# Performance work log

Hardware: AMD Instinct MI355X
Metric: run time of the kernel (lower is better)

The kernel has to match this reference:

```python
import jax, jax.numpy as jnp
import numpy as np

S = 2048      # seq_len
H = 32        # num_heads
G = 8         # num_groups (KV heads)
D = 128       # head_dim
HPG = H // G  # heads per group
MODEL = H * D


def setup_inputs() -> dict:
    rng = jax.random.key(0)
    ks = jax.random.split(rng, 6)
    return {
        "query": jax.random.normal(ks[0], (S, H, D), jnp.float32),
        "key":   jax.random.normal(ks[1], (S, G, D), jnp.float32),
        "value": jax.random.normal(ks[2], (S, G, D), jnp.float32),
        "mask":  jnp.zeros((S, S), jnp.float32),
        "w_out": jax.random.normal(ks[3], (MODEL, MODEL), jnp.float32) * (MODEL ** -0.5),
        "b_out": jnp.zeros((MODEL,), jnp.float32),
    }


def reference(query, key, value, mask, w_out, b_out):
    # NOTE: the original torch module prepares `mask` but never applies it to
    # the attention scores; we faithfully reproduce that (mask is unused).
    scale = D ** -0.5
    # [S,H,D] -> [H,S,D] -> [G,HPG,S,D]; head h = g*HPG + i (torch .view split)
    q = query.transpose(1, 0, 2).reshape(G, HPG, S, D)
    k = key.transpose(1, 0, 2)    # [G,S,D]
    v = value.transpose(1, 0, 2)  # [G,S,D]
    scores = jnp.einsum('ghqd,gkd->ghqk', q, k) * scale  # [G,HPG,S,S]
    attn = jax.nn.softmax(scores, axis=-1)
    out = jnp.einsum('ghqk,gkd->ghqd', attn, v)          # [G,HPG,S,D]
    # [G,HPG,S,D] -> [H,S,D] -> [S,H,D] -> [S, H*D]
    out = out.reshape(H, S, D).transpose(1, 0, 2).reshape(S, MODEL)
    out = out @ w_out.T + b_out                           # out_proj (Linear)
    return out.reshape(S, H, D)
```

## Files before the change

### kernel.cpp

```cpp
#include <hip/hip_runtime.h>
#include <hip/hip_bf16.h>
#include <stdint.h>

constexpr int S_ = 2048, H_ = 32, G_ = 8, HPG_ = 4, D_ = 128, MODEL_ = 4096;

typedef __attribute__((ext_vector_type(4))) float f32x4;
typedef __attribute__((ext_vector_type(16))) float f32x16;
typedef __attribute__((ext_vector_type(8))) short bf16x8;
typedef __attribute__((ext_vector_type(4))) short bf16x4;

__device__ inline unsigned short f2bf(float f) {
  unsigned u = __float_as_uint(f);
  u += 0x7FFFu + ((u >> 16) & 1u);
  return (unsigned short)(u >> 16);
}

__device__ inline unsigned cvt_pk_bf16(float lo, float hi) {
  unsigned r;
  asm("v_cvt_pk_bf16_f32 %0, %1, %2" : "=v"(r) : "v"(lo), "v"(hi));
  return r;
}

__device__ inline void gload_lds16(const void* g, void* l) {
  __builtin_amdgcn_global_load_lds(
      (const __attribute__((address_space(1))) unsigned int*)g,
      (__attribute__((address_space(3))) unsigned int*)l,
      16, 0, 0);
}

__global__ __launch_bounds__(256) void cvt_f32_to_bf16(
    const float* __restrict__ in, unsigned short* __restrict__ out, int n4) {
  int i = blockIdx.x * 256 + threadIdx.x;
  if (i < n4) {
    float4 v = reinterpret_cast<const float4*>(in)[i];
    bf16x4 o;
    o[0] = f2bf(v.x); o[1] = f2bf(v.y); o[2] = f2bf(v.z); o[3] = f2bf(v.w);
    reinterpret_cast<bf16x4*>(out)[i] = o;
  }
}

__global__ __launch_bounds__(256) void cvt_k_kernel(
    const float* __restrict__ in, unsigned short* __restrict__ out) {
  int i = blockIdx.x * 256 + threadIdx.x;
  int d4 = i & 31, g = (i >> 5) & 7, s = i >> 8;
  float4 v = reinterpret_cast<const float4*>(in)[i];
  bf16x4 o;
  o[0] = f2bf(v.x); o[1] = f2bf(v.y); o[2] = f2bf(v.z); o[3] = f2bf(v.w);
  reinterpret_cast<bf16x4*>(out)[(g * S_ + s) * 32 + d4] = o;
}

__global__ __launch_bounds__(256) void cvt_v_kernel(
    const float* __restrict__ in, unsigned short* __restrict__ out) {
  __shared__ float t[64][33];
  int s0 = blockIdx.x * 64, d0 = blockIdx.y * 32, g = blockIdx.z;
  int tid = threadIdx.x;
#pragma unroll
  for (int p = 0; p < 2; ++p) {
    int idx = p * 256 + tid;
    int s = idx >> 3, dq = (idx & 7) * 4;
    float4 v = *reinterpret_cast<const float4*>(
        in + ((size_t)(s0 + s) * G_ + g) * D_ + d0 + dq);
    t[s][dq] = v.x; t[s][dq + 1] = v.y; t[s][dq + 2] = v.z; t[s][dq + 3] = v.w;
  }
  __syncthreads();
  int d = tid >> 3, sq = (tid & 7) * 8;
  bf16x8 o;
#pragma unroll
  for (int j = 0; j < 8; ++j) o[j] = f2bf(t[sq + j][d]);
  *reinterpret_cast<bf16x8*>(out + ((size_t)g * D_ + d0 + d) * S_ + s0 + sq) = o;
}

constexpr int QB2 = 128, KVB = 32, NT = S_ / KVB;
constexpr float RTHR = 8.0f;

__global__ __launch_bounds__(256, 2) void attn32_kernel(
    const float* __restrict__ q, const unsigned short* __restrict__ kb,
    const unsigned short* __restrict__ vtb, unsigned short* __restrict__ aout) {
  __shared__ __align__(16) char smem[49152];

  const int qt = blockIdx.x, h = blockIdx.y;
  const int g = h >> 2;
  const int tid = threadIdx.x, w = tid >> 6, lane = tid & 63;
  const int l31 = lane & 31, hi = lane >> 5;

  const float scale = 0.08838834764831845f;
  bf16x8 qf[8];
  const int qrow = qt * QB2 + w * 32 + l31;
  {
    const float* qp = q + ((size_t)qrow * H_ + h) * D_;
#pragma unroll
    for (int c = 0; c < 8; ++c) {
      const float* p0 = qp + c * 16 + hi * 8;
      float4 a = *(const float4*)p0;
      float4 b = *(const float4*)(p0 + 4);
      bf16x8 f;
      f[0] = f2bf(a.x * scale); f[1] = f2bf(a.y * scale);
      f[2] = f2bf(a.z * scale); f[3] = f2bf(a.w * scale);
      f[4] = f2bf(b.x * scale); f[5] = f2bf(b.y * scale);
      f[6] = f2bf(b.z * scale); f[7] = f2bf(b.w * scale);
      qf[c] = f;
    }
  }

  int ks_kv[2], ks_d[2], vs_d[2], vs_kv[2];
#pragma unroll
  for (int hh = 0; hh < 2; ++hh) {
    int p = w * 1024 + hh * 4096 + lane * 16;
    int kvr = p >> 8;
    ks_kv[hh] = kvr;
    ks_d[hh] = ((p & 255) ^ ((kvr & 7) << 4)) >> 1;
    int dr = p >> 6;
    vs_d[hh] = dr;
    vs_kv[hh] = ((p & 63) ^ (((dr >> 1) & 3) << 4)) >> 1;
  }
  const unsigned short* kg = kb + (size_t)g * S_ * D_;
  const unsigned short* vg = vtb + (size_t)g * D_ * S_;

  auto stage = [&](int t, int buf) {
    int kv0 = t * KVB;
    char* Kd = smem + buf * 16384;
    char* Vd = smem + buf * 16384 + 8192;
#pragma unroll
    for (int hh = 0; hh < 2; ++hh) {
      gload_lds16(kg + (size_t)(kv0 + ks_kv[hh]) * D_ + ks_d[hh],
                  Kd + w * 1024 + hh * 4096);
      gload_lds16(vg + (size_t)vs_d[hh] * S_ + kv0 + vs_kv[hh],
                  Vd + w * 1024 + hh * 4096);
    }
  };

  f32x16 of[4];
#pragma unroll
  for (int i = 0; i < 4; ++i) of[i] = (f32x16)0.f;
  float m = -1e30f, l = 0.f;

  stage(0, 0);
  stage(1, 1);

  for (int t = 0; t < NT; ++t) {
    const int buf = t % 3;
    if (t + 1 < NT) asm volatile("s_waitcnt vmcnt(4)" ::: "memory");
    else            asm volatile("s_waitcnt vmcnt(0)" ::: "memory");
    __builtin_amdgcn_s_barrier();
    if (t + 2 < NT) stage(t + 2, (t + 2) % 3);

    const char* Kd = smem + buf * 16384;
    const char* Vd = smem + buf * 16384 + 8192;

    f32x16 s0 = (f32x16)0.f, s1 = (f32x16)0.f;
    __builtin_amdgcn_s_setprio(1);
#pragma unroll
    for (int c = 0; c < 8; ++c) {
      unsigned off = ((unsigned)(l31 * 256 + c * 32 + hi * 16)) ^
                     ((unsigned)(l31 & 7) << 4);
      bf16x8 kf = *(const bf16x8*)(Kd + off);
      if (c & 1)
        s1 = __builtin_amdgcn_mfma_f32_32x32x16_bf16(kf, qf[c], s1, 0, 0, 0);
      else
        s0 = __builtin_amdgcn_mfma_f32_32x32x16_bf16(kf, qf[c], s0, 0, 0, 0);
    }
    __builtin_amdgcn_s_setprio(0);
    f32x16 sv = s0 + s1;

    float tmax = sv[0];
#pragma unroll
    for (int r = 1; r < 16; ++r) tmax = fmaxf(tmax, sv[r]);
    tmax = fmaxf(tmax, __shfl_xor(tmax, 32));
    if (__any(tmax > m + RTHR)) {
      float mnew = fmaxf(m, tmax);
      float alpha = __expf(m - mnew);
#pragma unroll
      for (int i = 0; i < 4; ++i)
#pragma unroll
        for (int r = 0; r < 16; ++r) of[i][r] *= alpha;
      l *= alpha;
      m = mnew;
    }
    float pv[16];
    float sum = 0.f;
#pragma unroll
    for (int r = 0; r < 16; ++r) { pv[r] = __expf(sv[r] - m); sum += pv[r]; }
    sum += __shfl_xor(sum, 32);
    l += sum;

    unsigned pk[8];
#pragma unroll
    for (int b = 0; b < 8; ++b) pk[b] = cvt_pk_bf16(pv[2 * b], pv[2 * b + 1]);
    bf16x8 pf[2];
#pragma unroll
    for (int kc = 0; kc < 2; ++kc) {
      auto sA = __builtin_amdgcn_permlane32_swap(pk[kc * 4 + 0], pk[kc * 4 + 2],
                                                 false, false);
      auto sB = __builtin_amdgcn_permlane32_swap(pk[kc * 4 + 1], pk[kc * 4 + 3],
                                                 false, false);
      unsigned fr[4] = {(unsigned)sA[0], (unsigned)sB[0],
                        (unsigned)sA[1], (unsigned)sB[1]};
      __builtin_memcpy(&pf[kc], fr, 16);
    }

    __builtin_amdgcn_s_setprio(1);
#pragma unroll
    for (int db = 0; db < 4; ++db) {
      int d = db * 32 + l31;
#pragma unroll
      for (int kc = 0; kc < 2; ++kc) {
        unsigned off = ((unsigned)(d * 64 + kc * 32 + hi * 16)) ^
                       ((unsigned)((d >> 1) & 3) << 4);
        bf16x8 vf = *(const bf16x8*)(Vd + off);
        of[db] = __builtin_amdgcn_mfma_f32_32x32x16_bf16(vf, pf[kc], of[db], 0, 0, 0);
      }
    }
    __builtin_amdgcn_s_setprio(0);
  }

  __syncthreads();
  float inv = 1.0f / l;
  unsigned short* Ol = (unsigned short*)smem;
  const int ql = w * 32 + l31;
#pragma unroll
  for (int db = 0; db < 4; ++db) {
#pragma unroll
    for (int rp = 0; rp < 8; ++rp) {
      int r0 = rp * 2;
      int d0 = db * 32 + (r0 & 3) + 8 * (r0 >> 2) + 4 * hi;
      unsigned pkv = cvt_pk_bf16(of[db][r0] * inv, of[db][r0 + 1] * inv);
      unsigned off = ((unsigned)(ql * 256 + d0 * 2)) ^ ((unsigned)(ql & 7) << 4);
      *(unsigned*)((char*)Ol + off) = pkv;
    }
  }
  __syncthreads();
  const size_t obase = ((size_t)qt * QB2) * MODEL_ + (size_t)h * D_;
#pragma unroll
  for (int pass = 0; pass < 8; ++pass) {
    int row = pass * 16 + (tid >> 4);
    int c = tid & 15;
    unsigned off = ((unsigned)(row * 256 + c * 16)) ^ ((unsigned)(row & 7) << 4);
    bf16x8 vv = *(const bf16x8*)((char*)Ol + off);
    *(bf16x8*)(aout + obase + (size_t)row * MODEL_ + c * 8) = vv;
  }
}

constexpr int BM = 128, BN = 128, BK = 64;

__global__ __launch_bounds__(256, 2) void gemm_bt_bias(
    const unsigned short* __restrict__ A, const unsigned short* __restrict__ B,
    const float* __restrict__ bias, float* __restrict__ C) {
  __shared__ unsigned short As[BM * BK];
  __shared__ unsigned short Bs[BN * BK];

  const int tid = threadIdx.x;
  const int w = tid >> 6, lane = tid & 63;
  const int wr = w >> 1, wc = w & 1;
  const int r16 = lane & 15, g4 = lane >> 4;
  const int row0 = blockIdx.y * BM, col0 = blockIdx.x * BN;

  f32x4 acc[4][4];
#pragma unroll
  for (int m = 0; m < 4; ++m)
#pragma unroll
    for (int n = 0; n < 4; ++n) acc[m][n] = (f32x4)0.f;

  for (int kt = 0; kt < MODEL_ / BK; ++kt) {
    const int k0 = kt * BK;
    __syncthreads();
#pragma unroll
    for (int j = 0; j < 4; ++j) {
      int chunk = w * 4 + j;
      int sb = chunk * 1024 + lane * 16;
      int srow = sb >> 7;
      int lb = sb ^ ((srow & 7) << 4);
      int kk = (lb & 127) >> 1;
      gload_lds16(A + (size_t)(row0 + srow) * MODEL_ + k0 + kk,
                  (char*)As + chunk * 1024);
      gload_lds16(B + (size_t)(col0 + srow) * MODEL_ + k0 + kk,
                  (char*)Bs + chunk * 1024);
    }
    asm volatile("s_waitcnt vmcnt(0)" ::: "memory");
    __syncthreads();

#pragma unroll
    for (int kc = 0; kc < 2; ++kc) {
      bf16x8 af[4], bfr[4];
#pragma unroll
      for (int m = 0; m < 4; ++m) {
        int row = wr * 64 + m * 16 + r16;
        unsigned off = ((unsigned)(row * 128 + (kc * 32 + g4 * 8) * 2)) ^ ((row & 7) << 4);
        af[m] = *(bf16x8*)((char*)As + off);
      }
#pragma unroll
      for (int n = 0; n < 4; ++n) {
        int row = wc * 64 + n * 16 + r16;
        unsigned off = ((unsigned)(row * 128 + (kc * 32 + g4 * 8) * 2)) ^ ((row & 7) << 4);
        bfr[n] = *(bf16x8*)((char*)Bs + off);
      }
#pragma unroll
      for (int m = 0; m < 4; ++m)
#pragma unroll
        for (int n = 0; n < 4; ++n)
          acc[m][n] = __builtin_amdgcn_mfma_f32_16x16x32_bf16(af[m], bfr[n], acc[m][n], 0, 0, 0);
    }
  }

#pragma unroll
  for (int n = 0; n < 4; ++n) {
    int col = col0 + wc * 64 + n * 16 + r16;
    float bv = bias[col];
#pragma unroll
    for (int m = 0; m < 4; ++m) {
      int rbase = row0 + wr * 64 + m * 16 + g4 * 4;
#pragma unroll
      for (int j = 0; j < 4; ++j)
        C[(size_t)(rbase + j) * MODEL_ + col] = acc[m][n][j] + bv;
    }
  }
}

extern "C" void kernel_launch(void* const* d_in, const int* in_sizes, int n_in,
                              void* d_out, int out_size, void* d_ws, size_t ws_size,
                              hipStream_t stream) {
  const float* q = (const float*)d_in[0];
  const float* k = (const float*)d_in[1];
  const float* v = (const float*)d_in[2];
  const float* w_out = (const float*)d_in[4];
  const float* b_out = (const float*)d_in[5];
  float* out = (float*)d_out;

  unsigned short* attn_bf = (unsigned short*)d_ws;
  unsigned short* xreg = attn_bf + (size_t)S_ * MODEL_;
  unsigned short* k_bf = xreg;
  unsigned short* vt_bf = xreg + (size_t)G_ * S_ * D_;
  unsigned short* w_bf = xreg;
  if (ws_size < ((size_t)S_ * MODEL_ + (size_t)MODEL_ * MODEL_) * 2) return;

  cvt_k_kernel<<<S_ * G_ * D_ / 4 / 256, 256, 0, stream>>>(k, k_bf);
  dim3 vg(S_ / 64, D_ / 32, G_);
  cvt_v_kernel<<<vg, 256, 0, stream>>>(v, vt_bf);

  dim3 ag(S_ / QB2, H_);
  attn32_kernel<<<ag, 256, 0, stream>>>(q, k_bf, vt_bf, attn_bf);

  cvt_f32_to_bf16<<<(MODEL_ * MODEL_ / 4) / 256, 256, 0, stream>>>(
      w_out, w_bf, MODEL_ * MODEL_ / 4);

  dim3 gg(MODEL_ / BN, S_ / BM);
  gemm_bt_bias<<<gg, 256, 0, stream>>>(attn_bf, w_bf, b_out, out);
}
```

Baseline: 185.5 us.

## Software-pipeline QK MFMA one tile ahead and use exp2 softmax

Restructures the attention main loop so the QK^T MFMAs for tile t+1 are issued before the softmax and PV work of tile t, letting matrix ops overlap with the exp and max VALU work. The log2(e) factor is folded into the Q scale so the softmax can use exp2 directly. Max and sum reductions become tree-shaped to shorten dependency chains. In exchange it keeps an extra set of score accumulators live, adding register pressure, and the loop now waits on vmcnt(0) every iteration, which may expose more load latency.

```diff
diff --git a/kernel.cpp b/kernel.cpp
--- a/kernel.cpp
+++ b/kernel.cpp
@@ -83,7 +83,7 @@
   const int tid = threadIdx.x, w = tid >> 6, lane = tid & 63;
   const int l31 = lane & 31, hi = lane >> 5;
 
-  const float scale = 0.08838834764831845f;
+  const float scale2 = 0.12751742354783493f;
   bf16x8 qf[8];
   const int qrow = qt * QB2 + w * 32 + l31;
   {
@@ -94,10 +94,10 @@
       float4 a = *(const float4*)p0;
       float4 b = *(const float4*)(p0 + 4);
       bf16x8 f;
-      f[0] = f2bf(a.x * scale); f[1] = f2bf(a.y * scale);
-      f[2] = f2bf(a.z * scale); f[3] = f2bf(a.w * scale);
-      f[4] = f2bf(b.x * scale); f[5] = f2bf(b.y * scale);
-      f[6] = f2bf(b.z * scale); f[7] = f2bf(b.w * scale);
+      f[0] = f2bf(a.x * scale2); f[1] = f2bf(a.y * scale2);
+      f[2] = f2bf(a.z * scale2); f[3] = f2bf(a.w * scale2);
+      f[4] = f2bf(b.x * scale2); f[5] = f2bf(b.y * scale2);
+      f[6] = f2bf(b.z * scale2); f[7] = f2bf(b.w * scale2);
       qf[c] = f;
     }
   }
@@ -129,25 +129,7 @@
     }
   };
 
-  f32x16 of[4];
-#pragma unroll
-  for (int i = 0; i < 4; ++i) of[i] = (f32x16)0.f;
-  float m = -1e30f, l = 0.f;
-
-  stage(0, 0);
-  stage(1, 1);
-
-  for (int t = 0; t < NT; ++t) {
-    const int buf = t % 3;
-    if (t + 1 < NT) asm volatile("s_waitcnt vmcnt(4)" ::: "memory");
-    else            asm volatile("s_waitcnt vmcnt(0)" ::: "memory");
-    __builtin_amdgcn_s_barrier();
-    if (t + 2 < NT) stage(t + 2, (t + 2) % 3);
-
-    const char* Kd = smem + buf * 16384;
-    const char* Vd = smem + buf * 16384 + 8192;
-
-    f32x16 s0 = (f32x16)0.f, s1 = (f32x16)0.f;
+  auto qk_mfma = [&](const char* Kd, f32x16& a0, f32x16& a1) {
     __builtin_amdgcn_s_setprio(1);
 #pragma unroll
     for (int c = 0; c < 8; ++c) {
@@ -155,20 +137,47 @@
                      ((unsigned)(l31 & 7) << 4);
       bf16x8 kf = *(const bf16x8*)(Kd + off);
       if (c & 1)
-        s1 = __builtin_amdgcn_mfma_f32_32x32x16_bf16(kf, qf[c], s1, 0, 0, 0);
+        a1 = __builtin_amdgcn_mfma_f32_32x32x16_bf16(kf, qf[c], a1, 0, 0, 0);
       else
-        s0 = __builtin_amdgcn_mfma_f32_32x32x16_bf16(kf, qf[c], s0, 0, 0, 0);
+        a0 = __builtin_amdgcn_mfma_f32_32x32x16_bf16(kf, qf[c], a0, 0, 0, 0);
     }
     __builtin_amdgcn_s_setprio(0);
+  };
+
+  f32x16 of[4];
+#pragma unroll
+  for (int i = 0; i < 4; ++i) of[i] = (f32x16)0.f;
+  float m = -1e30f, l = 0.f;
+
+  stage(0, 0);
+  stage(1, 1);
+  asm volatile("s_waitcnt vmcnt(4)" ::: "memory");
+  __builtin_amdgcn_s_barrier();
+
+  f32x16 s0 = (f32x16)0.f, s1 = (f32x16)0.f;
+  qk_mfma(smem, s0, s1);
+
+  for (int t = 0; t < NT; ++t) {
+    asm volatile("s_waitcnt vmcnt(0)" ::: "memory");
+    __builtin_amdgcn_s_barrier();
+    if (t + 2 < NT) stage(t + 2, (t + 2) % 3);
+
     f32x16 sv = s0 + s1;
-
-    float tmax = sv[0];
-#pragma unroll
-    for (int r = 1; r < 16; ++r) tmax = fmaxf(tmax, sv[r]);
+    if (t + 1 < NT) {
+      s0 = (f32x16)0.f; s1 = (f32x16)0.f;
+      qk_mfma(smem + ((t + 1) % 3) * 16384, s0, s1);
+    }
+
+    float mx8[8];
+#pragma unroll
+    for (int i = 0; i < 8; ++i) mx8[i] = fmaxf(sv[i], sv[i + 8]);
+#pragma unroll
+    for (int i = 0; i < 4; ++i) mx8[i] = fmaxf(mx8[i], mx8[i + 4]);
+    float tmax = fmaxf(fmaxf(mx8[0], mx8[1]), fmaxf(mx8[2], mx8[3]));
     tmax = fmaxf(tmax, __shfl_xor(tmax, 32));
     if (__any(tmax > m + RTHR)) {
       float mnew = fmaxf(m, tmax);
-      float alpha = __expf(m - mnew);
+      float alpha = __builtin_exp2f(m - mnew);
 #pragma unroll
       for (int i = 0; i < 4; ++i)
 #pragma unroll
@@ -176,10 +185,14 @@
       l *= alpha;
       m = mnew;
     }
-    float pv[16];
-    float sum = 0.f;
-#pragma unroll
-    for (int r = 0; r < 16; ++r) { pv[r] = __expf(sv[r] - m); sum += pv[r]; }
+    float pv[16], ps[8];
+#pragma unroll
+    for (int r = 0; r < 16; ++r) pv[r] = __builtin_exp2f(sv[r] - m);
+#pragma unroll
+    for (int i = 0; i < 8; ++i) ps[i] = pv[i] + pv[i + 8];
+#pragma unroll
+    for (int i = 0; i < 4; ++i) ps[i] += ps[i + 4];
+    float sum = (ps[0] + ps[1]) + (ps[2] + ps[3]);
     sum += __shfl_xor(sum, 32);
     l += sum;
 
@@ -198,6 +211,7 @@
       __builtin_memcpy(&pf[kc], fr, 16);
     }
 
+    const char* Vd = smem + (t % 3) * 16384 + 8192;
     __builtin_amdgcn_s_setprio(1);
 #pragma unroll
     for (int db = 0; db < 4; ++db) {
```

Result: slower. 194.9 us (+5.1%).
